# Kernel optimization log

Measured on AMD Instinct MI355X. Metric: run time of the kernel, lower is better.

Reference implementation:

```python
import jax, jax.numpy as jnp
import numpy as np

SIGMA = 1.0

def setup_inputs() -> dict:
    key = jax.random.key(0)
    k1, k2 = jax.random.split(key)
    z = jax.random.normal(k1, (8192, 1024), dtype=jnp.float32)
    expert_keys = jax.random.normal(k2, (4096, 1024), dtype=jnp.float32)
    return {"z": z, "expert_keys": expert_keys}

def reference(z, expert_keys):
    # squared euclidean distances [N, E] = |z|^2 + |e|^2 - 2 z.e
    z_sq = jnp.sum(z * z, axis=-1, keepdims=True)          # [N, 1]
    e_sq = jnp.sum(expert_keys * expert_keys, axis=-1)     # [E]
    dist2 = z_sq + e_sq[None, :] - 2.0 * (z @ expert_keys.T)
    dist2 = jnp.maximum(dist2, 0.0)
    similarity = jnp.exp(-dist2 / (2.0 * SIGMA ** 2))       # [N, E]
    weights = jax.nn.softmax(similarity, axis=-1)            # [N, E]
    weighted_expert = weights @ expert_keys                  # [N, D]
    return (similarity, weighted_expert)
```

## Files before the change

### kernel.cpp

```cpp
#include <hip/hip_runtime.h>
#include <stdint.h>


#define M_TOK 8192
#define N_EXP 4096
#define D_DIM 1024

typedef __attribute__((ext_vector_type(4))) float f32x4;
typedef __attribute__((ext_vector_type(8))) short short8;
typedef __attribute__((ext_vector_type(4))) unsigned short u16x4;
typedef unsigned short u16;
typedef unsigned int u32;

__device__ __forceinline__ u16 f32_to_bf16(float f) {
  u32 u = __builtin_bit_cast(u32, f);
  u += 0x7fff + ((u >> 16) & 1);
  return (u16)(u >> 16);
}

__device__ __forceinline__ void async16(const void* g, void* l) {
  __builtin_amdgcn_global_load_lds((__attribute__((address_space(1))) void*)(g),
                                   (__attribute__((address_space(3))) void*)(l),
                                   16, 0, 0);
}

__global__ __launch_bounds__(256) void prep_convert2(const float* __restrict__ zsrc,
                                                     const float* __restrict__ esrc,
                                                     u16* __restrict__ zdst,
                                                     u16* __restrict__ edst,
                                                     float* __restrict__ zsq,
                                                     float* __restrict__ esq) {
  int row = blockIdx.x;
  const float* src;
  u16* dst;
  float* sq;
  if (row < M_TOK) {
    src = zsrc + (size_t)row * D_DIM;
    dst = zdst + (size_t)row * D_DIM;
    sq = zsq + row;
  } else {
    int r = row - M_TOK;
    src = esrc + (size_t)r * D_DIM;
    dst = edst + (size_t)r * D_DIM;
    sq = esq + r;
  }
  int t = threadIdx.x;
  const float4 v = ((const float4*)src)[t];
  ushort4 h;
  h.x = f32_to_bf16(v.x); h.y = f32_to_bf16(v.y);
  h.z = f32_to_bf16(v.z); h.w = f32_to_bf16(v.w);
  ((ushort4*)dst)[t] = h;
  float p = v.x * v.x + v.y * v.y + v.z * v.z + v.w * v.w;
#pragma unroll
  for (int off = 1; off < 64; off <<= 1) p += __shfl_xor(p, off, 64);
  __shared__ float partial[4];
  if ((t & 63) == 0) partial[t >> 6] = p;
  __syncthreads();
  if (t == 0) *sq = partial[0] + partial[1] + partial[2] + partial[3];
}

__global__ __launch_bounds__(256) void transpose_bf16(const u16* __restrict__ src,
                                                      u16* __restrict__ dst) {
  __shared__ u16 tile[64][65];
  int e0 = blockIdx.x * 64;
  int d0 = blockIdx.y * 64;
  int t = threadIdx.x;
  int lr = t >> 4;
  int lc = (t & 15) * 4;
#pragma unroll
  for (int r8 = 0; r8 < 4; ++r8) {
    int row = lr + r8 * 16;
    ushort4 v = *(const ushort4*)(src + (size_t)(e0 + row) * D_DIM + d0 + lc);
    tile[row][lc + 0] = v.x; tile[row][lc + 1] = v.y;
    tile[row][lc + 2] = v.z; tile[row][lc + 3] = v.w;
  }
  __syncthreads();
#pragma unroll
  for (int r8 = 0; r8 < 4; ++r8) {
    int dl = lr + r8 * 16;
    ushort4 v;
    v.x = tile[lc + 0][dl]; v.y = tile[lc + 1][dl];
    v.z = tile[lc + 2][dl]; v.w = tile[lc + 3][dl];
    *(ushort4*)(dst + (size_t)(d0 + dl) * N_EXP + e0 + lc) = v;
  }
}

__global__ __launch_bounds__(256) void rowsum_reduce(const float* __restrict__ part,
                                                     float* __restrict__ rowsum) {
  int r = blockIdx.x * 256 + threadIdx.x;
  float s = 0.f;
#pragma unroll 8
  for (int j = 0; j < 128; ++j) s += part[(size_t)j * M_TOK + r];
  rowsum[r] = s;
}

template <int EPI>
__global__ __launch_bounds__(512, 4) void gemm_bt(const u16* __restrict__ A,
                                                  const u16* __restrict__ Bt,
                                                  int Mdim, int Ndim, int Kdim,
                                                  float* __restrict__ out, int ldo,
                                                  const float* __restrict__ a_sq,
                                                  const float* __restrict__ b_sq,
                                                  float* __restrict__ rs_part,
                                                  u16* __restrict__ wb,
                                                  const float* __restrict__ scale) {
  constexpr int BM = 128, BN = 128, BK = 64;
  __shared__ __align__(16) u16 smA[2 * BM * BK];
  __shared__ __align__(16) u16 smB[2 * BN * BK];

  const int wg = blockIdx.x;
  int m0, n0, ntile = 0;
  if (EPI == 1) {
    const int xcd = wg & 7;
    const int idx = wg >> 3;
    const int sup = idx >> 5;
    const int mloc = (idx & 31) >> 2;
    const int nloc = idx & 3;
    m0 = (xcd * 8 + mloc) * BM;
    ntile = sup * 4 + nloc;
    n0 = ntile * BN;
  } else {
    const int nTilesN = Ndim / BN;
    const int nwg = (Mdim / BM) * nTilesN;
    const int cpx = nwg >> 3;
    const int swz = (wg & 7) * cpx + (wg >> 3);
    m0 = (swz / nTilesN) * BM;
    n0 = (swz % nTilesN) * BN;
  }

  const int t = threadIdx.x;
  const int l = t & 63;
  const int w = t >> 6;
  const int wr = w >> 2;
  const int wc = w & 3;
  const int lr8 = l >> 3;
  const int cswz = (((l & 7) ^ lr8) << 3);
  const int s0 = w * 2, s1 = w * 2 + 1;
  const int str0 = s0 * 8 + lr8, str1 = s1 * 8 + lr8;

  f32x4 acc[4][2];
#pragma unroll
  for (int i = 0; i < 4; ++i)
#pragma unroll
    for (int j = 0; j < 2; ++j) acc[i][j] = (f32x4){0.f, 0.f, 0.f, 0.f};

  const int nIter = Kdim / BK;
  async16(A + (size_t)(m0 + str0) * Kdim + cswz, smA + s0 * 512);
  async16(A + (size_t)(m0 + str1) * Kdim + cswz, smA + s1 * 512);
  async16(Bt + (size_t)(n0 + str0) * Kdim + cswz, smB + s0 * 512);
  async16(Bt + (size_t)(n0 + str1) * Kdim + cswz, smB + s1 * 512);
  __syncthreads();

  int cur = 0;
  for (int it = 0; it < nIter; ++it) {
    if (it + 1 < nIter) {
      const int k0 = (it + 1) * BK;
      const int nb = (cur ^ 1) * 8192;
      async16(A + (size_t)(m0 + str0) * Kdim + k0 + cswz, smA + nb + s0 * 512);
      async16(A + (size_t)(m0 + str1) * Kdim + k0 + cswz, smA + nb + s1 * 512);
      async16(Bt + (size_t)(n0 + str0) * Kdim + k0 + cswz, smB + nb + s0 * 512);
      async16(Bt + (size_t)(n0 + str1) * Kdim + k0 + cswz, smB + nb + s1 * 512);
    }
    const int cbase = cur * 8192;
#pragma unroll
    for (int ks = 0; ks < 2; ++ks) {
      short8 af[4], bf[2];
      const int lrow = l & 15;
      const int kb = ks * 64 + ((l >> 4) << 4);
#pragma unroll
      for (int mi = 0; mi < 4; ++mi) {
        int row = wr * 64 + mi * 16 + lrow;
        int addr = row * 128 + (kb ^ ((row & 7) << 4));
        af[mi] = *(const short8*)(smA + cbase + (addr >> 1));
      }
#pragma unroll
      for (int ni = 0; ni < 2; ++ni) {
        int row = wc * 32 + ni * 16 + lrow;
        int addr = row * 128 + (kb ^ ((row & 7) << 4));
        bf[ni] = *(const short8*)(smB + cbase + (addr >> 1));
      }
#pragma unroll
      for (int mi = 0; mi < 4; ++mi)
#pragma unroll
        for (int ni = 0; ni < 2; ++ni)
          acc[mi][ni] = __builtin_amdgcn_mfma_f32_16x16x32_bf16(
              bf[ni], af[mi], acc[mi][ni], 0, 0, 0);
    }
    __syncthreads();
    cur ^= 1;
  }

  const int lcol = l & 15;
  const int rgrp = l >> 4;
  if (EPI == 1) {
    float* ldsT = ((float*)smA) + w * (16 * 36);
    const int rr = l >> 3;
    const int c4 = (l & 7) * 4;
    const int slot = ntile * 4 + wc;
#pragma unroll
    for (int mi = 0; mi < 4; ++mi) {
      int grow = m0 + wr * 64 + mi * 16 + lcol;
      float zq = a_sq[grow];
#pragma unroll
      for (int ni = 0; ni < 2; ++ni) {
        int ncol = n0 + wc * 32 + ni * 16 + rgrp * 4;
        f32x4 eqv = *(const f32x4*)(b_sq + ncol);
        f32x4 simv;
#pragma unroll
        for (int r = 0; r < 4; ++r) {
          float dist2 = fmaxf(zq + eqv[r] - 2.0f * acc[mi][ni][r], 0.0f);
          simv[r] = __expf(-0.5f * dist2);
        }
        *(f32x4*)(ldsT + lcol * 36 + ni * 16 + rgrp * 4) = simv;
      }
      asm volatile("s_waitcnt lgkmcnt(0)" ::: "memory");
#pragma unroll
      for (int pass = 0; pass < 2; ++pass) {
        int rrow = pass * 8 + rr;
        f32x4 sv = *(const f32x4*)(ldsT + rrow * 36 + c4);
        int growr = m0 + wr * 64 + mi * 16 + rrow;
        size_t gbase = (size_t)growr * ldo + (n0 + wc * 32 + c4);
        __builtin_nontemporal_store(sv, (f32x4*)(out + gbase));
        f32x4 es;
#pragma unroll
        for (int r = 0; r < 4; ++r) es[r] = __expf(sv[r]);
        if (wb) {
          u16x4 wv;
          wv.x = f32_to_bf16(es[0]); wv.y = f32_to_bf16(es[1]);
          wv.z = f32_to_bf16(es[2]); wv.w = f32_to_bf16(es[3]);
          *(u16x4*)(wb + gbase) = wv;
        }
        float p = es[0] + es[1] + es[2] + es[3];
        p += __shfl_xor(p, 1, 64);
        p += __shfl_xor(p, 2, 64);
        p += __shfl_xor(p, 4, 64);
        if ((l & 7) == 0) rs_part[(size_t)slot * M_TOK + growr] = p;
      }
    }
  } else {
#pragma unroll
    for (int mi = 0; mi < 4; ++mi) {
      int grow = m0 + wr * 64 + mi * 16 + lcol;
      float s = scale ? (1.0f / scale[grow]) : 1.0f;
#pragma unroll
      for (int ni = 0; ni < 2; ++ni) {
        int ncol = n0 + wc * 32 + ni * 16 + rgrp * 4;
        f32x4 v = acc[mi][ni] * s;
        *(f32x4*)(out + (size_t)grow * ldo + ncol) = v;
      }
    }
  }
}

__global__ __launch_bounds__(256) void weights_kernel(const float* __restrict__ sim,
                                                      const float* __restrict__ rowsum,
                                                      u16* __restrict__ wb) {
  size_t i = ((size_t)blockIdx.x * 256 + threadIdx.x) * 8;
  int row = (int)(i >> 12);
  float inv = 1.0f / rowsum[row];
  float4 a = *(const float4*)(sim + i);
  float4 b = *(const float4*)(sim + i + 4);
  u32 w0 = (u32)f32_to_bf16(__expf(a.x) * inv) | ((u32)f32_to_bf16(__expf(a.y) * inv) << 16);
  u32 w1 = (u32)f32_to_bf16(__expf(a.z) * inv) | ((u32)f32_to_bf16(__expf(a.w) * inv) << 16);
  u32 w2 = (u32)f32_to_bf16(__expf(b.x) * inv) | ((u32)f32_to_bf16(__expf(b.y) * inv) << 16);
  u32 w3 = (u32)f32_to_bf16(__expf(b.z) * inv) | ((u32)f32_to_bf16(__expf(b.w) * inv) << 16);
  uint4 o; o.x = w0; o.y = w1; o.z = w2; o.w = w3;
  *(uint4*)(wb + i) = o;
}

extern "C" void kernel_launch(void* const* d_in, const int* in_sizes, int n_in,
                              void* d_out, int out_size, void* d_ws, size_t ws_size,
                              hipStream_t stream) {
  const float* z = (const float*)d_in[0];
  const float* e = (const float*)d_in[1];
  float* out = (float*)d_out;
  float* sim = out;
  float* wout = out + (size_t)M_TOK * N_EXP;

  char* ws = (char*)d_ws;
  const size_t MB = (size_t)1 << 20;
  const bool fused = ws_size >= 100 * MB + 96 * 1024;

  if (fused) {
    u16* zb  = (u16*)ws;
    u16* eb  = (u16*)(ws + 16 * MB);
    u16* ebT = (u16*)(ws + 24 * MB);
    u16* Wb  = (u16*)(ws + 32 * MB);
    float* rs_part = (float*)(ws + 96 * MB);
    float* z_sq   = (float*)(ws + 100 * MB);
    float* e_sq   = (float*)(ws + 100 * MB + 32768);
    float* rowsum = (float*)(ws + 100 * MB + 49152);

    prep_convert2<<<M_TOK + N_EXP, 256, 0, stream>>>(z, e, zb, eb, z_sq, e_sq);
    transpose_bf16<<<dim3(N_EXP / 64, D_DIM / 64), 256, 0, stream>>>(eb, ebT);

    gemm_bt<1><<<(M_TOK / 128) * (N_EXP / 128), 512, 0, stream>>>(
        zb, eb, M_TOK, N_EXP, D_DIM, sim, N_EXP, z_sq, e_sq, rs_part, Wb, nullptr);

    rowsum_reduce<<<M_TOK / 256, 256, 0, stream>>>(rs_part, rowsum);

    gemm_bt<0><<<(M_TOK / 128) * (D_DIM / 128), 512, 0, stream>>>(
        Wb, ebT, M_TOK, D_DIM, N_EXP, wout, D_DIM, nullptr, nullptr, nullptr,
        nullptr, rowsum);
  } else {
    u16* Wb  = (u16*)ws;
    u16* zb  = (u16*)ws;
    u16* eb  = (u16*)(ws + 64 * MB);
    u16* ebT = (u16*)(ws + 72 * MB);
    float* rs_part = (float*)(ws + 80 * MB);
    float* z_sq   = (float*)(ws + 84 * MB);
    float* e_sq   = (float*)(ws + 84 * MB + 32768);
    float* rowsum = (float*)(ws + 84 * MB + 49152);

    prep_convert2<<<M_TOK + N_EXP, 256, 0, stream>>>(z, e, zb, eb, z_sq, e_sq);
    transpose_bf16<<<dim3(N_EXP / 64, D_DIM / 64), 256, 0, stream>>>(eb, ebT);

    gemm_bt<1><<<(M_TOK / 128) * (N_EXP / 128), 512, 0, stream>>>(
        zb, eb, M_TOK, N_EXP, D_DIM, sim, N_EXP, z_sq, e_sq, rs_part, nullptr, nullptr);

    rowsum_reduce<<<M_TOK / 256, 256, 0, stream>>>(rs_part, rowsum);

    weights_kernel<<<(M_TOK * (size_t)N_EXP) / (8 * 256), 256, 0, stream>>>(sim, rowsum, Wb);

    gemm_bt<0><<<(M_TOK / 128) * (D_DIM / 128), 512, 0, stream>>>(
        Wb, ebT, M_TOK, D_DIM, N_EXP, wout, D_DIM, nullptr, nullptr, nullptr,
        nullptr, nullptr);
  }
}
```

Baseline: 187.9 us.

## Move softmax exp/rowsum out of GEMM epilogue into separate row pass kernel

Removes the exp, bf16 weight write and partial-rowsum shuffle from the first GEMM's epilogue, and switches its similarity store from nontemporal to a normal store. A new per-row kernel rereads the similarity matrix, computes exp, writes unnormalized bf16 weights and the row sum in one pass. The second GEMM then scales by the reciprocal row sum. This unfuses work to lighten the GEMM epilogue, but adds a full 128MB reread of the similarity matrix plus an extra launch.

```diff
diff --git a/kernel.cpp b/kernel.cpp
--- a/kernel.cpp
+++ b/kernel.cpp
@@ -8,7 +8,6 @@
 
 typedef __attribute__((ext_vector_type(4))) float f32x4;
 typedef __attribute__((ext_vector_type(8))) short short8;
-typedef __attribute__((ext_vector_type(4))) unsigned short u16x4;
 typedef unsigned short u16;
 typedef unsigned int u32;
 
@@ -85,13 +84,42 @@
   }
 }
 
-__global__ __launch_bounds__(256) void rowsum_reduce(const float* __restrict__ part,
-                                                     float* __restrict__ rowsum) {
-  int r = blockIdx.x * 256 + threadIdx.x;
-  float s = 0.f;
-#pragma unroll 8
-  for (int j = 0; j < 128; ++j) s += part[(size_t)j * M_TOK + r];
-  rowsum[r] = s;
+__global__ __launch_bounds__(256) void espass(const float* __restrict__ sim,
+                                              u16* __restrict__ wb,
+                                              float* __restrict__ rowsum) {
+  const int row = blockIdx.x;
+  const float* sp = sim + (size_t)row * N_EXP;
+  u16* wp = wb + (size_t)row * N_EXP;
+  const int t = threadIdx.x;
+  const int base = t * 16;
+  f32x4 v0 = *(const f32x4*)(sp + base);
+  f32x4 v1 = *(const f32x4*)(sp + base + 4);
+  f32x4 v2 = *(const f32x4*)(sp + base + 8);
+  f32x4 v3 = *(const f32x4*)(sp + base + 12);
+  f32x4 e0, e1, e2, e3;
+#pragma unroll
+  for (int r = 0; r < 4; ++r) {
+    e0[r] = __expf(v0[r]); e1[r] = __expf(v1[r]);
+    e2[r] = __expf(v2[r]); e3[r] = __expf(v3[r]);
+  }
+  short8 lo, hi;
+#pragma unroll
+  for (int r = 0; r < 4; ++r) {
+    lo[r]     = (short)f32_to_bf16(e0[r]);
+    lo[r + 4] = (short)f32_to_bf16(e1[r]);
+    hi[r]     = (short)f32_to_bf16(e2[r]);
+    hi[r + 4] = (short)f32_to_bf16(e3[r]);
+  }
+  *(short8*)(wp + base) = lo;
+  *(short8*)(wp + base + 8) = hi;
+  float p = (e0[0] + e0[1] + e0[2] + e0[3]) + (e1[0] + e1[1] + e1[2] + e1[3]) +
+            (e2[0] + e2[1] + e2[2] + e2[3]) + (e3[0] + e3[1] + e3[2] + e3[3]);
+#pragma unroll
+  for (int off = 1; off < 64; off <<= 1) p += __shfl_xor(p, off, 64);
+  __shared__ float partial[4];
+  if ((t & 63) == 0) partial[t >> 6] = p;
+  __syncthreads();
+  if (t == 0) rowsum[row] = partial[0] + partial[1] + partial[2] + partial[3];
 }
 
 template <int EPI>
@@ -101,15 +129,13 @@
                                                   float* __restrict__ out, int ldo,
                                                   const float* __restrict__ a_sq,
                                                   const float* __restrict__ b_sq,
-                                                  float* __restrict__ rs_part,
-                                                  u16* __restrict__ wb,
                                                   const float* __restrict__ scale) {
   constexpr int BM = 128, BN = 128, BK = 64;
   __shared__ __align__(16) u16 smA[2 * BM * BK];
   __shared__ __align__(16) u16 smB[2 * BN * BK];
 
   const int wg = blockIdx.x;
-  int m0, n0, ntile = 0;
+  int m0, n0;
   if (EPI == 1) {
     const int xcd = wg & 7;
     const int idx = wg >> 3;
@@ -117,8 +143,7 @@
     const int mloc = (idx & 31) >> 2;
     const int nloc = idx & 3;
     m0 = (xcd * 8 + mloc) * BM;
-    ntile = sup * 4 + nloc;
-    n0 = ntile * BN;
+    n0 = (sup * 4 + nloc) * BN;
   } else {
     const int nTilesN = Ndim / BN;
     const int nwg = (Mdim / BM) * nTilesN;
@@ -196,7 +221,6 @@
     float* ldsT = ((float*)smA) + w * (16 * 36);
     const int rr = l >> 3;
     const int c4 = (l & 7) * 4;
-    const int slot = ntile * 4 + wc;
 #pragma unroll
     for (int mi = 0; mi < 4; ++mi) {
       int grow = m0 + wr * 64 + mi * 16 + lcol;
@@ -220,21 +244,7 @@
         f32x4 sv = *(const f32x4*)(ldsT + rrow * 36 + c4);
         int growr = m0 + wr * 64 + mi * 16 + rrow;
         size_t gbase = (size_t)growr * ldo + (n0 + wc * 32 + c4);
-        __builtin_nontemporal_store(sv, (f32x4*)(out + gbase));
-        f32x4 es;
-#pragma unroll
-        for (int r = 0; r < 4; ++r) es[r] = __expf(sv[r]);
-        if (wb) {
-          u16x4 wv;
-          wv.x = f32_to_bf16(es[0]); wv.y = f32_to_bf16(es[1]);
-          wv.z = f32_to_bf16(es[2]); wv.w = f32_to_bf16(es[3]);
-          *(u16x4*)(wb + gbase) = wv;
-        }
-        float p = es[0] + es[1] + es[2] + es[3];
-        p += __shfl_xor(p, 1, 64);
-        p += __shfl_xor(p, 2, 64);
-        p += __shfl_xor(p, 4, 64);
-        if ((l & 7) == 0) rs_part[(size_t)slot * M_TOK + growr] = p;
+        *(f32x4*)(out + gbase) = sv;
       }
     }
   } else {
@@ -250,22 +260,6 @@
       }
     }
   }
-}
-
-__global__ __launch_bounds__(256) void weights_kernel(const float* __restrict__ sim,
-                                                      const float* __restrict__ rowsum,
-                                                      u16* __restrict__ wb) {
-  size_t i = ((size_t)blockIdx.x * 256 + threadIdx.x) * 8;
-  int row = (int)(i >> 12);
-  float inv = 1.0f / rowsum[row];
-  float4 a = *(const float4*)(sim + i);
-  float4 b = *(const float4*)(sim + i + 4);
-  u32 w0 = (u32)f32_to_bf16(__expf(a.x) * inv) | ((u32)f32_to_bf16(__expf(a.y) * inv) << 16);
-  u32 w1 = (u32)f32_to_bf16(__expf(a.z) * inv) | ((u32)f32_to_bf16(__expf(a.w) * inv) << 16);
-  u32 w2 = (u32)f32_to_bf16(__expf(b.x) * inv) | ((u32)f32_to_bf16(__expf(b.y) * inv) << 16);
-  u32 w3 = (u32)f32_to_bf16(__expf(b.z) * inv) | ((u32)f32_to_bf16(__expf(b.w) * inv) << 16);
-  uint4 o; o.x = w0; o.y = w1; o.z = w2; o.w = w3;
-  *(uint4*)(wb + i) = o;
 }
 
 extern "C" void kernel_launch(void* const* d_in, const int* in_sizes, int n_in,
@@ -279,51 +273,35 @@
 
   char* ws = (char*)d_ws;
   const size_t MB = (size_t)1 << 20;
-  const bool fused = ws_size >= 100 * MB + 96 * 1024;
-
-  if (fused) {
-    u16* zb  = (u16*)ws;
-    u16* eb  = (u16*)(ws + 16 * MB);
-    u16* ebT = (u16*)(ws + 24 * MB);
-    u16* Wb  = (u16*)(ws + 32 * MB);
-    float* rs_part = (float*)(ws + 96 * MB);
-    float* z_sq   = (float*)(ws + 100 * MB);
-    float* e_sq   = (float*)(ws + 100 * MB + 32768);
-    float* rowsum = (float*)(ws + 100 * MB + 49152);
-
-    prep_convert2<<<M_TOK + N_EXP, 256, 0, stream>>>(z, e, zb, eb, z_sq, e_sq);
-    transpose_bf16<<<dim3(N_EXP / 64, D_DIM / 64), 256, 0, stream>>>(eb, ebT);
-
-    gemm_bt<1><<<(M_TOK / 128) * (N_EXP / 128), 512, 0, stream>>>(
-        zb, eb, M_TOK, N_EXP, D_DIM, sim, N_EXP, z_sq, e_sq, rs_part, Wb, nullptr);
-
-    rowsum_reduce<<<M_TOK / 256, 256, 0, stream>>>(rs_part, rowsum);
-
-    gemm_bt<0><<<(M_TOK / 128) * (D_DIM / 128), 512, 0, stream>>>(
-        Wb, ebT, M_TOK, D_DIM, N_EXP, wout, D_DIM, nullptr, nullptr, nullptr,
-        nullptr, rowsum);
+
+  u16 *zb, *eb, *ebT, *Wb;
+  float *z_sq, *e_sq, *rowsum;
+  if (ws_size >= 96 * MB + 80 * 1024) {
+    zb  = (u16*)ws;
+    eb  = (u16*)(ws + 16 * MB);
+    ebT = (u16*)(ws + 24 * MB);
+    Wb  = (u16*)(ws + 32 * MB);
+    z_sq   = (float*)(ws + 96 * MB);
+    e_sq   = (float*)(ws + 96 * MB + 32768);
+    rowsum = (float*)(ws + 96 * MB + 49152);
   } else {
-    u16* Wb  = (u16*)ws;
-    u16* zb  = (u16*)ws;
-    u16* eb  = (u16*)(ws + 64 * MB);
-    u16* ebT = (u16*)(ws + 72 * MB);
-    float* rs_part = (float*)(ws + 80 * MB);
-    float* z_sq   = (float*)(ws + 84 * MB);
-    float* e_sq   = (float*)(ws + 84 * MB + 32768);
-    float* rowsum = (float*)(ws + 84 * MB + 49152);
-
-    prep_convert2<<<M_TOK + N_EXP, 256, 0, stream>>>(z, e, zb, eb, z_sq, e_sq);
-    transpose_bf16<<<dim3(N_EXP / 64, D_DIM / 64), 256, 0, stream>>>(eb, ebT);
-
-    gemm_bt<1><<<(M_TOK / 128) * (N_EXP / 128), 512, 0, stream>>>(
-        zb, eb, M_TOK, N_EXP, D_DIM, sim, N_EXP, z_sq, e_sq, rs_part, nullptr, nullptr);
-
-    rowsum_reduce<<<M_TOK / 256, 256, 0, stream>>>(rs_part, rowsum);
-
-    weights_kernel<<<(M_TOK * (size_t)N_EXP) / (8 * 256), 256, 0, stream>>>(sim, rowsum, Wb);
-
-    gemm_bt<0><<<(M_TOK / 128) * (D_DIM / 128), 512, 0, stream>>>(
-        Wb, ebT, M_TOK, D_DIM, N_EXP, wout, D_DIM, nullptr, nullptr, nullptr,
-        nullptr, nullptr);
-  }
-}
+    Wb  = (u16*)ws;
+    zb  = (u16*)ws;
+    eb  = (u16*)(ws + 64 * MB);
+    ebT = (u16*)(ws + 72 * MB);
+    z_sq   = (float*)(ws + 80 * MB);
+    e_sq   = (float*)(ws + 80 * MB + 32768);
+    rowsum = (float*)(ws + 80 * MB + 49152);
+  }
+
+  prep_convert2<<<M_TOK + N_EXP, 256, 0, stream>>>(z, e, zb, eb, z_sq, e_sq);
+  transpose_bf16<<<dim3(N_EXP / 64, D_DIM / 64), 256, 0, stream>>>(eb, ebT);
+
+  gemm_bt<1><<<(M_TOK / 128) * (N_EXP / 128), 512, 0, stream>>>(
+      zb, eb, M_TOK, N_EXP, D_DIM, sim, N_EXP, z_sq, e_sq, nullptr);
+
+  espass<<<M_TOK, 256, 0, stream>>>(sim, Wb, rowsum);
+
+  gemm_bt<0><<<(M_TOK / 128) * (D_DIM / 128), 512, 0, stream>>>(
+      Wb, ebT, M_TOK, D_DIM, N_EXP, wout, D_DIM, nullptr, nullptr, rowsum);
+}
```

After: 200.9 us. 1.07x slower.
